# Kernel tuning notes

Hardware: AMD Instinct MI355X
Metric: run time of the kernel (lower is better)

Reference implementation:

```python
import jax, jax.numpy as jnp
import numpy as np

K, B, S, D, V, H = 4, 64, 50, 256, 40000, 4
DH = D // H
TOPK = 2
NEG = -1e9
SCALE = float(1.0 / np.sqrt(DH))


def setup_inputs() -> dict:
    key = jax.random.key(0)
    ks = jax.random.split(key, 16)
    s = 0.05
    return {
        "ids":   jax.random.randint(ks[0], (K, B, S), 0, V),
        "items": jax.random.randint(ks[1], (K, B, S), 0, V),
        "adj":   jax.random.randint(ks[2], (B, S, S), 0, 5),
        "alias": jax.random.randint(ks[3], (B, S), 0, S),
        "eps":   jax.random.normal(ks[4], (B, S, K), jnp.float32),
        "emb":   jax.random.normal(ks[5], (K, V, D), jnp.float32) * s,
        "agg_a": jax.random.normal(ks[6], (K, 4, D), jnp.float32) * s,
        "Wq": jax.random.normal(ks[7], (K, D, D), jnp.float32) * s,
        "Wk": jax.random.normal(ks[8], (K, D, D), jnp.float32) * s,
        "Wv": jax.random.normal(ks[9], (K, D, D), jnp.float32) * s,
        "Wo": jax.random.normal(ks[10], (K, D, D), jnp.float32) * s,
        "ln1_g": jnp.ones((K, D), jnp.float32),
        "ln1_b": jnp.zeros((K, D), jnp.float32),
        "W1": jax.random.normal(ks[11], (K, D, 4 * D), jnp.float32) * s,
        "W2": jax.random.normal(ks[12], (K, 4 * D, D), jnp.float32) * s,
        "ln2_g": jnp.ones((K, D), jnp.float32),
        "ln2_b": jnp.zeros((K, D), jnp.float32),
        "Wg": jax.random.normal(ks[13], (D, K), jnp.float32) * s,
        "Wn": jax.random.normal(ks[14], (D, K), jnp.float32) * s,
    }


def _layer_norm(x, g, b):
    m = jnp.mean(x, -1, keepdims=True)
    v = jnp.var(x, -1, keepdims=True)
    return (x - m) * jax.lax.rsqrt(v + 1e-5) * g + b


def _per_key(ids, items, emb, a, Wq, Wk, Wv, Wo, g1, b1, W1, W2, g2, b2, adj, alias):
    hg = emb[items]                                          # [B,S,D] graph-node embeddings
    # LocalAggregator: relation-typed pairwise attention over session graph (adj in {1..4})
    e = jnp.einsum('bid,bjd,rd->rbij', hg, hg, a)            # [4,B,S,S], avoids [B,S,S,D]
    e = jax.nn.leaky_relu(e, 0.2)
    alpha = jnp.full(adj.shape, NEG, e.dtype)
    for r in range(4):
        alpha = jnp.where(adj == r + 1, e[r], alpha)
    alpha = jax.nn.softmax(alpha, -1)
    h_local = jnp.einsum('bij,bjd->bid', alpha, hg)          # graph aggregation
    h = jnp.take_along_axis(h_local, alias[..., None], axis=1)   # distribute graph rows to sequence
    # memory-transformer block (pre-LN causal MHA + FFN)
    x = _layer_norm(h, g1, b1)
    q = (x @ Wq).reshape(B, S, H, DH)
    k = (x @ Wk).reshape(B, S, H, DH)
    v = (x @ Wv).reshape(B, S, H, DH)
    scores = jnp.einsum('bihd,bjhd->bhij', q, k) * SCALE
    causal = jnp.tril(jnp.ones((S, S), bool))
    scores = jnp.where(causal, scores, NEG)
    attn = jax.nn.softmax(scores, -1)
    o = jnp.einsum('bhij,bjhd->bihd', attn, v).reshape(B, S, D) @ Wo
    h = h + o
    y = _layer_norm(h, g2, b2)
    h = h + jax.nn.gelu(y @ W1) @ W2
    return h


def reference(ids, items, adj, alias, eps, emb, agg_a, Wq, Wk, Wv, Wo,
              ln1_g, ln1_b, W1, W2, ln2_g, ln2_b, Wg, Wn):
    per_key = jax.vmap(_per_key, in_axes=(0,) * 14 + (None, None))
    h_keys = per_key(ids, items, emb, agg_a, Wq, Wk, Wv, Wo,
                     ln1_g, ln1_b, W1, W2, ln2_g, ln2_b, adj, alias)   # [K,B,S,D]
    # gate input: mean over per-key input-sequence embeddings (h_seq in original)
    h_seq = jax.vmap(lambda e, i: e[i])(emb, ids).mean(0)              # [B,S,D]
    # noisy top-k gating over node-type experts
    logits = h_seq @ Wg + jax.nn.softplus(h_seq @ Wn) * eps            # [B,S,K]
    top_v, top_i = jax.lax.top_k(logits, TOPK)
    w = jax.nn.softmax(top_v, -1)                                      # [B,S,TOPK]
    gates = jnp.sum(jax.nn.one_hot(top_i, K, dtype=w.dtype) * w[..., None], axis=-2)  # [B,S,K]
    return jnp.einsum('bsk,kbsd->bsd', gates, h_keys)
```

## Files before the change

### kernel.cpp

```cpp
#include <hip/hip_runtime.h>
#include <hip/hip_bf16.h>
#include <math.h>

#define K_ 4
#define B_ 64
#define S_ 50
#define D_ 256
#define V_ 40000
#define H_ 4
#define DH_ 64
#define NEG_ (-1e9f)
#define SCALE_ 0.125f

typedef __attribute__((ext_vector_type(8))) __bf16 bf16x8v;
typedef __attribute__((ext_vector_type(4))) float f32x4v;

__device__ __forceinline__ float wred_sum(float v) {
#pragma unroll
  for (int off = 32; off > 0; off >>= 1) v += __shfl_xor(v, off, 64);
  return v;
}
__device__ __forceinline__ float wred_max(float v) {
#pragma unroll
  for (int off = 32; off > 0; off >>= 1) v = fmaxf(v, __shfl_xor(v, off, 64));
  return v;
}
__device__ __forceinline__ float softplusf(float x) {
  return (x > 20.f) ? x : log1pf(expf(x));
}
__device__ __forceinline__ float geluf(float x) {
  const float c = 0.7978845608028654f;
  float x3 = x * x * x;
  return 0.5f * x * (1.f + tanhf(c * (x + 0.044715f * x3)));
}
__device__ __forceinline__ float bf2f(unsigned int u) {
  return __uint_as_float(u << 16);
}
__device__ __forceinline__ unsigned short f2bf(float f) {
  unsigned u = __float_as_uint(f);
  return (unsigned short)((u + 0x7fffu + ((u >> 16) & 1u)) >> 16);
}
__device__ __forceinline__ void unp8(uint4 a, float* d) {
  d[0] = bf2f(a.x & 0xffffu); d[1] = bf2f(a.x >> 16);
  d[2] = bf2f(a.y & 0xffffu); d[3] = bf2f(a.y >> 16);
  d[4] = bf2f(a.z & 0xffffu); d[5] = bf2f(a.z >> 16);
  d[6] = bf2f(a.w & 0xffffu); d[7] = bf2f(a.w >> 16);
}
__device__ __forceinline__ bf16x8v cvt8(float4 a, float4 b) {
  bf16x8v r;
  r[0] = (__bf16)a.x; r[1] = (__bf16)a.y; r[2] = (__bf16)a.z; r[3] = (__bf16)a.w;
  r[4] = (__bf16)b.x; r[5] = (__bf16)b.y; r[6] = (__bf16)b.z; r[7] = (__bf16)b.w;
  return r;
}

__global__ __launch_bounds__(256) void cast_weights(
    const float* __restrict__ wq, const float* __restrict__ wk,
    const float* __restrict__ wv, const float* __restrict__ wo,
    const float* __restrict__ w1, const float* __restrict__ w2,
    unsigned short* __restrict__ wqkvT, unsigned short* __restrict__ woT,
    unsigned short* __restrict__ w1T, unsigned short* __restrict__ w2T) {
  long i4 = ((long)blockIdx.x * 256 + threadIdx.x) * 4;
  if (i4 < 786432) {
    int sect = (int)(i4 / 262144);
    long e = i4 - (long)sect * 262144;
    const float* src = (sect == 0) ? wq : (sect == 1) ? wk : wv;
    int k = (int)(e >> 16), rem = (int)(e & 65535);
    int d = rem >> 8, n = rem & 255;
    float4 v = *(const float4*)(src + e);
    unsigned short* base = wqkvT + ((long)k * 768 + sect * 256 + n) * 256 + d;
    base[0] = f2bf(v.x); base[256] = f2bf(v.y);
    base[512] = f2bf(v.z); base[768] = f2bf(v.w);
    return;
  }
  if (i4 < 1048576) {
    long e = i4 - 786432;
    int k = (int)(e >> 16), rem = (int)(e & 65535);
    int d = rem >> 8, n = rem & 255;
    float4 v = *(const float4*)(wo + e);
    unsigned short* base = woT + ((long)k * 256 + n) * 256 + d;
    base[0] = f2bf(v.x); base[256] = f2bf(v.y);
    base[512] = f2bf(v.z); base[768] = f2bf(v.w);
    return;
  }
  if (i4 < 2097152) {
    long e = i4 - 1048576;
    int k = (int)(e >> 18), rem = (int)(e & 262143);
    int d = rem >> 10, n = rem & 1023;
    float4 v = *(const float4*)(w1 + e);
    unsigned short* base = w1T + ((long)k * 1024 + n) * 256 + d;
    base[0] = f2bf(v.x); base[256] = f2bf(v.y);
    base[512] = f2bf(v.z); base[768] = f2bf(v.w);
    return;
  }
  {
    long e = i4 - 2097152;
    int k = (int)(e >> 18), rem = (int)(e & 262143);
    int d = rem >> 8, n = rem & 255;
    float4 v = *(const float4*)(w2 + e);
    unsigned short* base = w2T + ((long)k * 256 + n) * 1024 + d;
    base[0] = f2bf(v.x); base[1024] = f2bf(v.y);
    base[2048] = f2bf(v.z); base[3072] = f2bf(v.w);
  }
}

__global__ __launch_bounds__(256) void gate_kernel(
    const int* __restrict__ ids, const float* __restrict__ emb,
    const float* __restrict__ Wg, const float* __restrict__ Wn,
    const float* __restrict__ eps, float* __restrict__ gates) {
  int w = threadIdx.x >> 6, lane = threadIdx.x & 63;
  int item = blockIdx.x * 4 + w;
  int b = item / S_, s = item % S_;
  int d0 = lane * 4;
  float4 hs = make_float4(0.f, 0.f, 0.f, 0.f);
#pragma unroll
  for (int k = 0; k < K_; ++k) {
    int id = ids[(k * B_ + b) * S_ + s];
    const float4 e = *(const float4*)(emb + ((long)k * V_ + id) * D_ + d0);
    hs.x += e.x; hs.y += e.y; hs.z += e.z; hs.w += e.w;
  }
  hs.x *= 0.25f; hs.y *= 0.25f; hs.z *= 0.25f; hs.w *= 0.25f;
  float logit[4];
#pragma unroll
  for (int j = 0; j < K_; ++j) {
    float pg = hs.x * Wg[(d0 + 0) * K_ + j] + hs.y * Wg[(d0 + 1) * K_ + j] +
               hs.z * Wg[(d0 + 2) * K_ + j] + hs.w * Wg[(d0 + 3) * K_ + j];
    float pn = hs.x * Wn[(d0 + 0) * K_ + j] + hs.y * Wn[(d0 + 1) * K_ + j] +
               hs.z * Wn[(d0 + 2) * K_ + j] + hs.w * Wn[(d0 + 3) * K_ + j];
    pg = wred_sum(pg);
    pn = wred_sum(pn);
    logit[j] = pg + softplusf(pn) * eps[item * K_ + j];
  }
  if (lane == 0) {
    int i0 = 0; float v0 = logit[0];
    for (int j = 1; j < K_; ++j) if (logit[j] > v0) { v0 = logit[j]; i0 = j; }
    int i1 = -1; float v1 = 0.f;
    for (int j = 0; j < K_; ++j)
      if (j != i0 && (i1 < 0 || logit[j] > v1)) { v1 = logit[j]; i1 = j; }
    float w0 = 1.f / (1.f + expf(v1 - v0));
    float w1 = 1.f - w0;
#pragma unroll
    for (int j = 0; j < K_; ++j)
      gates[item * K_ + j] = (j == i0) ? w0 : ((j == i1) ? w1 : 0.f);
  }
}

__global__ __launch_bounds__(256) void local_agg4(
    const int* __restrict__ items, const int* __restrict__ adj,
    const float* __restrict__ emb, const float* __restrict__ agg_a,
    float* __restrict__ h_raw) {
  __shared__ __bf16 hgb[64][264];
  __shared__ float e_f[50][68];
  __shared__ __bf16 alp[64][72];
  __shared__ unsigned char adj_s[64][64];
  __shared__ __bf16 a_sb[4][264];
  int kb = blockIdx.x;
  int k = kb >> 6, b = kb & 63;
  int t = threadIdx.x;
  for (int c = t; c < 2048; c += 256) {
    int row = c >> 5, c8 = (c & 31) * 8;
    bf16x8v val;
    if (row < S_) {
      int g = items[kb * S_ + row];
      const float* src = emb + ((long)k * V_ + g) * D_ + c8;
      val = cvt8(*(const float4*)src, *(const float4*)(src + 4));
    } else {
#pragma unroll
      for (int e = 0; e < 8; ++e) val[e] = (__bf16)0.f;
    }
    *(bf16x8v*)&hgb[row][c8] = val;
  }
  if (t < 128) {
    int row = t >> 5, c8 = (t & 31) * 8;
    const float* src = agg_a + ((long)k * 4 + row) * D_ + c8;
    *(bf16x8v*)&a_sb[row][c8] = cvt8(*(const float4*)src, *(const float4*)(src + 4));
  }
  for (int c = t; c < 4096; c += 256) {
    int i = c >> 6, j = c & 63;
    adj_s[i][j] = (i < S_ && j < S_)
                      ? (unsigned char)adj[((long)b * S_ + i) * S_ + j] : 0;
  }
  __syncthreads();
  int w = t >> 6, lane = t & 63;
  int m16 = lane & 15, quad = lane >> 4;
  float e_sel[4][4];
#pragma unroll
  for (int nt = 0; nt < 4; ++nt)
#pragma unroll
    for (int rg = 0; rg < 4; ++rg) e_sel[nt][rg] = NEG_;
#pragma unroll
  for (int r = 0; r < 4; ++r) {
    f32x4v acc[4];
#pragma unroll
    for (int nt = 0; nt < 4; ++nt) acc[nt] = (f32x4v){0.f, 0.f, 0.f, 0.f};
#pragma unroll
    for (int k0 = 0; k0 < 8; ++k0) {
      int kc = k0 * 32 + quad * 8;
      bf16x8v hr = *(const bf16x8v*)&hgb[w * 16 + m16][kc];
      bf16x8v ar = *(const bf16x8v*)&a_sb[r][kc];
      bf16x8v af;
#pragma unroll
      for (int e = 0; e < 8; ++e) af[e] = (__bf16)((float)hr[e] * (float)ar[e]);
#pragma unroll
      for (int nt = 0; nt < 4; ++nt) {
        bf16x8v bf = *(const bf16x8v*)&hgb[nt * 16 + m16][kc];
        acc[nt] = __builtin_amdgcn_mfma_f32_16x16x32_bf16(af, bf, acc[nt], 0, 0, 0);
      }
    }
#pragma unroll
    for (int nt = 0; nt < 4; ++nt)
#pragma unroll
      for (int rg = 0; rg < 4; ++rg) {
        int i = w * 16 + quad * 4 + rg, j = nt * 16 + m16;
        if (adj_s[i][j] == r + 1) {
          float v = acc[nt][rg];
          e_sel[nt][rg] = (v >= 0.f) ? v : 0.2f * v;
        }
      }
  }
#pragma unroll
  for (int nt = 0; nt < 4; ++nt)
#pragma unroll
    for (int rg = 0; rg < 4; ++rg) {
      int i = w * 16 + quad * 4 + rg;
      if (i < S_) e_f[i][nt * 16 + m16] = e_sel[nt][rg];
    }
  __syncthreads();
  for (int i = w; i < S_; i += 4) {
    float val = (lane < S_) ? e_f[i][lane] : -INFINITY;
    float m = wred_max(val);
    float p = expf(val - m);
    float ssum = wred_sum(p);
    alp[i][lane] = (__bf16)(p / ssum);
  }
  __syncthreads();
#pragma unroll 4
  for (int nt = 0; nt < 16; ++nt) {
    f32x4v acc = (f32x4v){0.f, 0.f, 0.f, 0.f};
#pragma unroll
    for (int k0 = 0; k0 < 2; ++k0) {
      int jb = k0 * 32 + quad * 8;
      bf16x8v af = *(const bf16x8v*)&alp[w * 16 + m16][jb];
      bf16x8v bf;
#pragma unroll
      for (int tt = 0; tt < 8; ++tt) bf[tt] = hgb[jb + tt][nt * 16 + m16];
      acc = __builtin_amdgcn_mfma_f32_16x16x32_bf16(af, bf, acc, 0, 0, 0);
    }
#pragma unroll
    for (int rg = 0; rg < 4; ++rg) {
      int i = w * 16 + quad * 4 + rg;
      if (i < S_)
        h_raw[((long)kb * S_ + i) * D_ + nt * 16 + m16] = acc[rg];
    }
  }
}

__global__ __launch_bounds__(256) void gather_ln(
    const float* __restrict__ h_raw, const int* __restrict__ alias_,
    float* __restrict__ hbuf, unsigned short* __restrict__ xb,
    const float* __restrict__ g, const float* __restrict__ bta) {
  int kb = blockIdx.x;
  int k = kb >> 6, b = kb & 63;
  int w = threadIdx.x >> 6, lane = threadIdx.x & 63;
  for (int s = w; s < S_; s += 4) {
    int src = alias_[b * S_ + s];
    const float4 v = *(const float4*)(h_raw + ((long)kb * S_ + src) * D_ + lane * 4);
    long off = ((long)kb * S_ + s) * D_ + lane * 4;
    *(float4*)(hbuf + off) = v;
    float sum = wred_sum(v.x + v.y + v.z + v.w);
    float sq = wred_sum(v.x * v.x + v.y * v.y + v.z * v.z + v.w * v.w);
    float mean = sum * (1.f / D_);
    float var = sq * (1.f / D_) - mean * mean;
    float rs = rsqrtf(var + 1e-5f);
    const float4 gv = *(const float4*)(g + k * D_ + lane * 4);
    const float4 bv = *(const float4*)(bta + k * D_ + lane * 4);
    ushort4 o;
    o.x = f2bf((v.x - mean) * rs * gv.x + bv.x);
    o.y = f2bf((v.y - mean) * rs * gv.y + bv.y);
    o.z = f2bf((v.z - mean) * rs * gv.z + bv.z);
    o.w = f2bf((v.w - mean) * rs * gv.w + bv.w);
    *(ushort4*)(xb + off) = o;
  }
}

__global__ __launch_bounds__(256) void ln_bf16(
    const float* __restrict__ x, unsigned short* __restrict__ y,
    const float* __restrict__ g, const float* __restrict__ bta) {
  int w = threadIdx.x >> 6, lane = threadIdx.x & 63;
  long row = (long)blockIdx.x * 4 + w;
  int k = (int)(row / (B_ * S_));
  const float4 v = *(const float4*)(x + row * D_ + lane * 4);
  float sum = wred_sum(v.x + v.y + v.z + v.w);
  float sq = wred_sum(v.x * v.x + v.y * v.y + v.z * v.z + v.w * v.w);
  float mean = sum * (1.f / D_);
  float var = sq * (1.f / D_) - mean * mean;
  float rs = rsqrtf(var + 1e-5f);
  const float4 gv = *(const float4*)(g + k * D_ + lane * 4);
  const float4 bv = *(const float4*)(bta + k * D_ + lane * 4);
  ushort4 o;
  o.x = f2bf((v.x - mean) * rs * gv.x + bv.x);
  o.y = f2bf((v.y - mean) * rs * gv.y + bv.y);
  o.z = f2bf((v.z - mean) * rs * gv.z + bv.z);
  o.w = f2bf((v.w - mean) * rs * gv.w + bv.w);
  *(ushort4*)(y + row * D_ + lane * 4) = o;
}

__global__ __launch_bounds__(256) void bgemm2(
    const unsigned short* __restrict__ A, const unsigned short* __restrict__ Bt,
    long strideA, long strideBt, int N, int Kd,
    float* __restrict__ Cf, long strideCf,
    const float* __restrict__ R, long strideR,
    unsigned short* __restrict__ Cb, long strideCb, int act) {
  __shared__ unsigned short sA[64][72];
  __shared__ unsigned short sB[64][72];
  int z = blockIdx.z;
  A += (long)z * strideA;
  Bt += (long)z * strideBt;
  int t = threadIdx.x, w = t >> 6, lane = t & 63;
  int row0 = blockIdx.x * 64, col0 = blockIdx.y * 64;
  int m16 = lane & 15, quad = lane >> 4;
  f32x4v acc[4];
#pragma unroll
  for (int nt = 0; nt < 4; ++nt) acc[nt] = (f32x4v){0.f, 0.f, 0.f, 0.f};
  int sr = t >> 2, sc = (t & 3) * 16;
  const unsigned short* pa = A + (long)(row0 + sr) * Kd + sc;
  const unsigned short* pb = Bt + (long)(col0 + sr) * Kd + sc;
  uint4 a0 = *(const uint4*)(pa);
  uint4 a1 = *(const uint4*)(pa + 8);
  uint4 b0 = *(const uint4*)(pb);
  uint4 b1 = *(const uint4*)(pb + 8);
  for (int k0 = 0; k0 < Kd; k0 += 64) {
    __syncthreads();
    *(uint4*)&sA[sr][sc] = a0;
    *(uint4*)&sA[sr][sc + 8] = a1;
    *(uint4*)&sB[sr][sc] = b0;
    *(uint4*)&sB[sr][sc + 8] = b1;
    if (k0 + 64 < Kd) {
      a0 = *(const uint4*)(pa + k0 + 64);
      a1 = *(const uint4*)(pa + k0 + 72);
      b0 = *(const uint4*)(pb + k0 + 64);
      b1 = *(const uint4*)(pb + k0 + 72);
    }
    __syncthreads();
#pragma unroll
    for (int half = 0; half < 2; ++half) {
      int kg = half * 32 + quad * 8;
      bf16x8v af = *(const bf16x8v*)&sA[w * 16 + m16][kg];
#pragma unroll
      for (int nt = 0; nt < 4; ++nt) {
        bf16x8v bf = *(const bf16x8v*)&sB[nt * 16 + m16][kg];
        acc[nt] = __builtin_amdgcn_mfma_f32_16x16x32_bf16(af, bf, acc[nt], 0, 0, 0);
      }
    }
  }
  int rbase = row0 + w * 16 + quad * 4;
  int cb = m16;
#pragma unroll
  for (int nt = 0; nt < 4; ++nt) {
#pragma unroll
    for (int i2 = 0; i2 < 4; ++i2) {
      long off = (long)(rbase + i2) * N + col0 + nt * 16 + cb;
      float vv = acc[nt][i2];
      if (R) vv += R[(long)z * strideR + off];
      if (act == 1) vv = geluf(vv);
      if (Cf) Cf[(long)z * strideCf + off] = vv;
      if (Cb) Cb[(long)z * strideCb + off] = f2bf(vv);
    }
  }
}

__global__ __launch_bounds__(256) void attn_kernel(
    const unsigned short* __restrict__ qkv, unsigned short* __restrict__ o) {
  __shared__ float qs[S_][65], ks[S_][65], vs[S_][65];
  int idx = blockIdx.x;
  int h = idx & 3;
  int kb = idx >> 2;
  long base = (long)kb * S_ * 768;
  int t = threadIdx.x;
  for (int f = t; f < S_ * 8; f += 256) {
    int row = f >> 3, c8 = (f & 7) * 8;
    long g = base + (long)row * 768 + h * DH_ + c8;
    unp8(*(const uint4*)(qkv + g), &qs[row][c8]);
    unp8(*(const uint4*)(qkv + g + 256), &ks[row][c8]);
    unp8(*(const uint4*)(qkv + g + 512), &vs[row][c8]);
  }
  __syncthreads();
  int w = t >> 6, lane = t & 63;
  for (int i = w; i < S_; i += 4) {
    int jj = (lane < S_) ? lane : 0;
    float dot = 0.f;
#pragma unroll
    for (int d = 0; d < DH_; ++d) dot = fmaf(qs[i][d], ks[jj][d], dot);
    float val = (lane <= i) ? dot * SCALE_ : ((lane < S_) ? NEG_ : -INFINITY);
    float m = wred_max(val);
    float p = expf(val - m);
    float ssum = wred_sum(p);
    float pr = p / ssum;
    float acc = 0.f;
    for (int j = 0; j <= i; ++j)
      acc = fmaf(__shfl(pr, j, 64), vs[j][lane], acc);
    o[((long)kb * S_ + i) * D_ + h * DH_ + lane] = f2bf(acc);
  }
}

__global__ __launch_bounds__(256) void combine_kernel(
    const float* __restrict__ gates, const float* __restrict__ h,
    float* __restrict__ out) {
  int w = threadIdx.x >> 6, lane = threadIdx.x & 63;
  int item = blockIdx.x * 4 + w;
  float g0 = gates[item * 4 + 0], g1 = gates[item * 4 + 1];
  float g2 = gates[item * 4 + 2], g3 = gates[item * 4 + 3];
  long off = (long)item * D_ + lane * 4;
  const long PK = (long)B_ * S_ * D_;
  float4 a = *(const float4*)(h + off);
  float4 b = *(const float4*)(h + PK + off);
  float4 c = *(const float4*)(h + 2 * PK + off);
  float4 d = *(const float4*)(h + 3 * PK + off);
  float4 o;
  o.x = g0 * a.x + g1 * b.x + g2 * c.x + g3 * d.x;
  o.y = g0 * a.y + g1 * b.y + g2 * c.y + g3 * d.y;
  o.z = g0 * a.z + g1 * b.z + g2 * c.z + g3 * d.z;
  o.w = g0 * a.w + g1 * b.w + g2 * c.w + g3 * d.w;
  *(float4*)(out + off) = o;
}

extern "C" void kernel_launch(void* const* d_in, const int* in_sizes, int n_in,
                              void* d_out, int out_size, void* d_ws,
                              size_t ws_size, hipStream_t stream) {
  const int* ids = (const int*)d_in[0];
  const int* items = (const int*)d_in[1];
  const int* adj = (const int*)d_in[2];
  const int* alias = (const int*)d_in[3];
  const float* eps = (const float*)d_in[4];
  const float* emb = (const float*)d_in[5];
  const float* agg_a = (const float*)d_in[6];
  const float* Wq = (const float*)d_in[7];
  const float* Wk = (const float*)d_in[8];
  const float* Wv = (const float*)d_in[9];
  const float* Wo = (const float*)d_in[10];
  const float* ln1g = (const float*)d_in[11];
  const float* ln1b = (const float*)d_in[12];
  const float* W1 = (const float*)d_in[13];
  const float* W2 = (const float*)d_in[14];
  const float* ln2g = (const float*)d_in[15];
  const float* ln2b = (const float*)d_in[16];
  const float* Wg = (const float*)d_in[17];
  const float* Wn = (const float*)d_in[18];
  float* out = (float*)d_out;

  const long BSD = (long)B_ * S_ * D_;
  float* ws = (float*)d_ws;
  float* gates = ws;
  float* hbuf = ws + 16384;
  unsigned short* ub = (unsigned short*)(ws + 16384 + 4 * BSD);
  unsigned short* xb = ub;
  unsigned short* qkvb = ub + 3276800;
  unsigned short* tb = qkvb;
  float* h_raw = (float*)qkvb;
  unsigned short* wqkvT = ub + 16384000;
  unsigned short* woT = wqkvT + 786432;
  unsigned short* w1T = woT + 262144;
  unsigned short* w2T = w1T + 1048576;

  const long T4 = 3276800;

  cast_weights<<<3072, 256, 0, stream>>>(Wq, Wk, Wv, Wo, W1, W2,
                                         wqkvT, woT, w1T, w2T);
  gate_kernel<<<800, 256, 0, stream>>>(ids, emb, Wg, Wn, eps, gates);
  local_agg4<<<256, 256, 0, stream>>>(items, adj, emb, agg_a, h_raw);
  gather_ln<<<256, 256, 0, stream>>>(h_raw, alias, hbuf, xb, ln1g, ln1b);
  bgemm2<<<dim3(50, 12, 4), 256, 0, stream>>>(xb, wqkvT, BSD, 196608, 768, 256,
      (float*)0, 0, (const float*)0, 0, qkvb, 2457600, 0);
  attn_kernel<<<K_ * B_ * H_, 256, 0, stream>>>(qkvb, xb);
  bgemm2<<<dim3(50, 4, 4), 256, 0, stream>>>(xb, woT, BSD, 65536, 256, 256,
      hbuf, BSD, hbuf, BSD, (unsigned short*)0, 0, 0);
  ln_bf16<<<3200, 256, 0, stream>>>(hbuf, xb, ln2g, ln2b);
  bgemm2<<<dim3(50, 16, 4), 256, 0, stream>>>(xb, w1T, BSD, 262144, 1024, 256,
      (float*)0, 0, (const float*)0, 0, tb, T4, 1);
  bgemm2<<<dim3(50, 4, 4), 256, 0, stream>>>(tb, w2T, T4, 262144, 256, 1024,
      hbuf, BSD, hbuf, BSD, (unsigned short*)0, 0, 0);
  combine_kernel<<<800, 256, 0, stream>>>(gates, hbuf, out);
}
```

Measured before the change: 439.0 us.

## Fuse front kernels, Wo GEMM with LayerNorm, and W2 GEMM with gating combine

Merges weight casting, gating and local aggregation into one multi-role front kernel. The weight transpose now goes through an LDS tile, so the bf16 stores are coalesced. The Wo projection is fused with the residual add and the second LayerNorm. The W2 GEMM now loops over the four experts and applies the gates directly, which removes the separate ln_bf16 and combine launches and their HBM round trips. The trade-off is fewer blocks (200) for the fused GEMMs, each doing more serial work, which may lower occupancy and parallelism.

```diff
diff --git a/kernel.cpp b/kernel.cpp
--- a/kernel.cpp
+++ b/kernel.cpp
@@ -53,203 +53,216 @@
   return r;
 }
 
-__global__ __launch_bounds__(256) void cast_weights(
+__global__ __launch_bounds__(256) void front_kernel(
+    const int* __restrict__ items, const int* __restrict__ adj,
+    const float* __restrict__ emb, const float* __restrict__ agg_a,
+    float* __restrict__ h_raw,
+    const int* __restrict__ ids, const float* __restrict__ Wg,
+    const float* __restrict__ Wn, const float* __restrict__ eps,
+    float* __restrict__ gates,
     const float* __restrict__ wq, const float* __restrict__ wk,
     const float* __restrict__ wv, const float* __restrict__ wo,
     const float* __restrict__ w1, const float* __restrict__ w2,
     unsigned short* __restrict__ wqkvT, unsigned short* __restrict__ woT,
     unsigned short* __restrict__ w1T, unsigned short* __restrict__ w2T) {
-  long i4 = ((long)blockIdx.x * 256 + threadIdx.x) * 4;
-  if (i4 < 786432) {
-    int sect = (int)(i4 / 262144);
-    long e = i4 - (long)sect * 262144;
-    const float* src = (sect == 0) ? wq : (sect == 1) ? wk : wv;
-    int k = (int)(e >> 16), rem = (int)(e & 65535);
-    int d = rem >> 8, n = rem & 255;
-    float4 v = *(const float4*)(src + e);
-    unsigned short* base = wqkvT + ((long)k * 768 + sect * 256 + n) * 256 + d;
-    base[0] = f2bf(v.x); base[256] = f2bf(v.y);
-    base[512] = f2bf(v.z); base[768] = f2bf(v.w);
-    return;
-  }
-  if (i4 < 1048576) {
-    long e = i4 - 786432;
-    int k = (int)(e >> 16), rem = (int)(e & 65535);
-    int d = rem >> 8, n = rem & 255;
-    float4 v = *(const float4*)(wo + e);
-    unsigned short* base = woT + ((long)k * 256 + n) * 256 + d;
-    base[0] = f2bf(v.x); base[256] = f2bf(v.y);
-    base[512] = f2bf(v.z); base[768] = f2bf(v.w);
-    return;
-  }
-  if (i4 < 2097152) {
-    long e = i4 - 1048576;
-    int k = (int)(e >> 18), rem = (int)(e & 262143);
-    int d = rem >> 10, n = rem & 1023;
-    float4 v = *(const float4*)(w1 + e);
-    unsigned short* base = w1T + ((long)k * 1024 + n) * 256 + d;
-    base[0] = f2bf(v.x); base[256] = f2bf(v.y);
-    base[512] = f2bf(v.z); base[768] = f2bf(v.w);
-    return;
-  }
-  {
-    long e = i4 - 2097152;
-    int k = (int)(e >> 18), rem = (int)(e & 262143);
-    int d = rem >> 8, n = rem & 255;
-    float4 v = *(const float4*)(w2 + e);
-    unsigned short* base = w2T + ((long)k * 256 + n) * 1024 + d;
-    base[0] = f2bf(v.x); base[1024] = f2bf(v.y);
-    base[2048] = f2bf(v.z); base[3072] = f2bf(v.w);
-  }
-}
-
-__global__ __launch_bounds__(256) void gate_kernel(
-    const int* __restrict__ ids, const float* __restrict__ emb,
-    const float* __restrict__ Wg, const float* __restrict__ Wn,
-    const float* __restrict__ eps, float* __restrict__ gates) {
-  int w = threadIdx.x >> 6, lane = threadIdx.x & 63;
-  int item = blockIdx.x * 4 + w;
-  int b = item / S_, s = item % S_;
-  int d0 = lane * 4;
-  float4 hs = make_float4(0.f, 0.f, 0.f, 0.f);
-#pragma unroll
-  for (int k = 0; k < K_; ++k) {
-    int id = ids[(k * B_ + b) * S_ + s];
-    const float4 e = *(const float4*)(emb + ((long)k * V_ + id) * D_ + d0);
-    hs.x += e.x; hs.y += e.y; hs.z += e.z; hs.w += e.w;
-  }
-  hs.x *= 0.25f; hs.y *= 0.25f; hs.z *= 0.25f; hs.w *= 0.25f;
-  float logit[4];
-#pragma unroll
-  for (int j = 0; j < K_; ++j) {
-    float pg = hs.x * Wg[(d0 + 0) * K_ + j] + hs.y * Wg[(d0 + 1) * K_ + j] +
-               hs.z * Wg[(d0 + 2) * K_ + j] + hs.w * Wg[(d0 + 3) * K_ + j];
-    float pn = hs.x * Wn[(d0 + 0) * K_ + j] + hs.y * Wn[(d0 + 1) * K_ + j] +
-               hs.z * Wn[(d0 + 2) * K_ + j] + hs.w * Wn[(d0 + 3) * K_ + j];
-    pg = wred_sum(pg);
-    pn = wred_sum(pn);
-    logit[j] = pg + softplusf(pn) * eps[item * K_ + j];
-  }
-  if (lane == 0) {
-    int i0 = 0; float v0 = logit[0];
-    for (int j = 1; j < K_; ++j) if (logit[j] > v0) { v0 = logit[j]; i0 = j; }
-    int i1 = -1; float v1 = 0.f;
-    for (int j = 0; j < K_; ++j)
-      if (j != i0 && (i1 < 0 || logit[j] > v1)) { v1 = logit[j]; i1 = j; }
-    float w0 = 1.f / (1.f + expf(v1 - v0));
-    float w1 = 1.f - w0;
-#pragma unroll
-    for (int j = 0; j < K_; ++j)
-      gates[item * K_ + j] = (j == i0) ? w0 : ((j == i1) ? w1 : 0.f);
-  }
-}
-
-__global__ __launch_bounds__(256) void local_agg4(
-    const int* __restrict__ items, const int* __restrict__ adj,
-    const float* __restrict__ emb, const float* __restrict__ agg_a,
-    float* __restrict__ h_raw) {
   __shared__ __bf16 hgb[64][264];
   __shared__ float e_f[50][68];
   __shared__ __bf16 alp[64][72];
   __shared__ unsigned char adj_s[64][64];
   __shared__ __bf16 a_sb[4][264];
-  int kb = blockIdx.x;
-  int k = kb >> 6, b = kb & 63;
+  int bid = blockIdx.x;
   int t = threadIdx.x;
-  for (int c = t; c < 2048; c += 256) {
-    int row = c >> 5, c8 = (c & 31) * 8;
-    bf16x8v val;
-    if (row < S_) {
-      int g = items[kb * S_ + row];
-      const float* src = emb + ((long)k * V_ + g) * D_ + c8;
-      val = cvt8(*(const float4*)src, *(const float4*)(src + 4));
+
+  if (bid < 256) {
+    int kb = bid;
+    int k = kb >> 6, b = kb & 63;
+    for (int c = t; c < 2048; c += 256) {
+      int row = c >> 5, c8 = (c & 31) * 8;
+      bf16x8v val;
+      if (row < S_) {
+        int g = items[kb * S_ + row];
+        const float* src = emb + ((long)k * V_ + g) * D_ + c8;
+        val = cvt8(*(const float4*)src, *(const float4*)(src + 4));
+      } else {
+#pragma unroll
+        for (int e = 0; e < 8; ++e) val[e] = (__bf16)0.f;
+      }
+      *(bf16x8v*)&hgb[row][c8] = val;
+    }
+    if (t < 128) {
+      int row = t >> 5, c8 = (t & 31) * 8;
+      const float* src = agg_a + ((long)k * 4 + row) * D_ + c8;
+      *(bf16x8v*)&a_sb[row][c8] = cvt8(*(const float4*)src, *(const float4*)(src + 4));
+    }
+    for (int c = t; c < 4096; c += 256) {
+      int i = c >> 6, j = c & 63;
+      adj_s[i][j] = (i < S_ && j < S_)
+                        ? (unsigned char)adj[((long)b * S_ + i) * S_ + j] : 0;
+    }
+    __syncthreads();
+    int w = t >> 6, lane = t & 63;
+    int m16 = lane & 15, quad = lane >> 4;
+    float e_sel[4][4];
+#pragma unroll
+    for (int nt = 0; nt < 4; ++nt)
+#pragma unroll
+      for (int rg = 0; rg < 4; ++rg) e_sel[nt][rg] = NEG_;
+#pragma unroll
+    for (int r = 0; r < 4; ++r) {
+      f32x4v acc[4];
+#pragma unroll
+      for (int nt = 0; nt < 4; ++nt) acc[nt] = (f32x4v){0.f, 0.f, 0.f, 0.f};
+#pragma unroll
+      for (int k0 = 0; k0 < 8; ++k0) {
+        int kc = k0 * 32 + quad * 8;
+        bf16x8v hr = *(const bf16x8v*)&hgb[w * 16 + m16][kc];
+        bf16x8v ar = *(const bf16x8v*)&a_sb[r][kc];
+        bf16x8v af;
+#pragma unroll
+        for (int e = 0; e < 8; ++e) af[e] = (__bf16)((float)hr[e] * (float)ar[e]);
+#pragma unroll
+        for (int nt = 0; nt < 4; ++nt) {
+          bf16x8v bf = *(const bf16x8v*)&hgb[nt * 16 + m16][kc];
+          acc[nt] = __builtin_amdgcn_mfma_f32_16x16x32_bf16(af, bf, acc[nt], 0, 0, 0);
+        }
+      }
+#pragma unroll
+      for (int nt = 0; nt < 4; ++nt)
+#pragma unroll
+        for (int rg = 0; rg < 4; ++rg) {
+          int i = w * 16 + quad * 4 + rg, j = nt * 16 + m16;
+          if (adj_s[i][j] == r + 1) {
+            float v = acc[nt][rg];
+            e_sel[nt][rg] = (v >= 0.f) ? v : 0.2f * v;
+          }
+        }
+    }
+#pragma unroll
+    for (int nt = 0; nt < 4; ++nt)
+#pragma unroll
+      for (int rg = 0; rg < 4; ++rg) {
+        int i = w * 16 + quad * 4 + rg;
+        if (i < S_) e_f[i][nt * 16 + m16] = e_sel[nt][rg];
+      }
+    __syncthreads();
+    for (int i = w; i < S_; i += 4) {
+      float val = (lane < S_) ? e_f[i][lane] : -INFINITY;
+      float m = wred_max(val);
+      float p = expf(val - m);
+      float ssum = wred_sum(p);
+      alp[i][lane] = (__bf16)(p / ssum);
+    }
+    __syncthreads();
+#pragma unroll 4
+    for (int nt = 0; nt < 16; ++nt) {
+      f32x4v acc = (f32x4v){0.f, 0.f, 0.f, 0.f};
+#pragma unroll
+      for (int k0 = 0; k0 < 2; ++k0) {
+        int jb = k0 * 32 + quad * 8;
+        bf16x8v af = *(const bf16x8v*)&alp[w * 16 + m16][jb];
+        bf16x8v bf;
+#pragma unroll
+        for (int tt = 0; tt < 8; ++tt) bf[tt] = hgb[jb + tt][nt * 16 + m16];
+        acc = __builtin_amdgcn_mfma_f32_16x16x32_bf16(af, bf, acc, 0, 0, 0);
+      }
+#pragma unroll
+      for (int rg = 0; rg < 4; ++rg) {
+        int i = w * 16 + quad * 4 + rg;
+        if (i < S_)
+          h_raw[((long)kb * S_ + i) * D_ + nt * 16 + m16] = acc[rg];
+      }
+    }
+    return;
+  }
+
+  if (bid < 1024) {
+    int tid = bid - 256;
+    typedef unsigned short row66[66];
+    row66* tile = (row66*)&hgb[0][0];
+    const float* src; unsigned short* dst; int C, R; int r0, c0;
+    if (tid < 192) {
+      int sect = tid >> 6; int rem = tid & 63;
+      int k = rem >> 4, t2 = rem & 15;
+      r0 = (t2 >> 2) * 64; c0 = (t2 & 3) * 64;
+      src = ((sect == 0) ? wq : (sect == 1) ? wk : wv) + (long)k * 65536;
+      dst = wqkvT + ((long)k * 768 + sect * 256) * 256;
+      R = 256; C = 256;
+    } else if (tid < 256) {
+      int rem = tid - 192; int k = rem >> 4, t2 = rem & 15;
+      r0 = (t2 >> 2) * 64; c0 = (t2 & 3) * 64;
+      src = wo + (long)k * 65536; dst = woT + (long)k * 65536;
+      R = 256; C = 256;
+    } else if (tid < 512) {
+      int rem = tid - 256; int k = rem >> 6, t2 = rem & 63;
+      r0 = (t2 >> 4) * 64; c0 = (t2 & 15) * 64;
+      src = w1 + (long)k * 262144; dst = w1T + (long)k * 262144;
+      R = 256; C = 1024;
     } else {
-#pragma unroll
-      for (int e = 0; e < 8; ++e) val[e] = (__bf16)0.f;
-    }
-    *(bf16x8v*)&hgb[row][c8] = val;
-  }
-  if (t < 128) {
-    int row = t >> 5, c8 = (t & 31) * 8;
-    const float* src = agg_a + ((long)k * 4 + row) * D_ + c8;
-    *(bf16x8v*)&a_sb[row][c8] = cvt8(*(const float4*)src, *(const float4*)(src + 4));
-  }
-  for (int c = t; c < 4096; c += 256) {
-    int i = c >> 6, j = c & 63;
-    adj_s[i][j] = (i < S_ && j < S_)
-                      ? (unsigned char)adj[((long)b * S_ + i) * S_ + j] : 0;
-  }
-  __syncthreads();
-  int w = t >> 6, lane = t & 63;
-  int m16 = lane & 15, quad = lane >> 4;
-  float e_sel[4][4];
-#pragma unroll
-  for (int nt = 0; nt < 4; ++nt)
-#pragma unroll
-    for (int rg = 0; rg < 4; ++rg) e_sel[nt][rg] = NEG_;
-#pragma unroll
-  for (int r = 0; r < 4; ++r) {
-    f32x4v acc[4];
-#pragma unroll
-    for (int nt = 0; nt < 4; ++nt) acc[nt] = (f32x4v){0.f, 0.f, 0.f, 0.f};
-#pragma unroll
-    for (int k0 = 0; k0 < 8; ++k0) {
-      int kc = k0 * 32 + quad * 8;
-      bf16x8v hr = *(const bf16x8v*)&hgb[w * 16 + m16][kc];
-      bf16x8v ar = *(const bf16x8v*)&a_sb[r][kc];
-      bf16x8v af;
-#pragma unroll
-      for (int e = 0; e < 8; ++e) af[e] = (__bf16)((float)hr[e] * (float)ar[e]);
-#pragma unroll
-      for (int nt = 0; nt < 4; ++nt) {
-        bf16x8v bf = *(const bf16x8v*)&hgb[nt * 16 + m16][kc];
-        acc[nt] = __builtin_amdgcn_mfma_f32_16x16x32_bf16(af, bf, acc[nt], 0, 0, 0);
-      }
-    }
-#pragma unroll
-    for (int nt = 0; nt < 4; ++nt)
-#pragma unroll
-      for (int rg = 0; rg < 4; ++rg) {
-        int i = w * 16 + quad * 4 + rg, j = nt * 16 + m16;
-        if (adj_s[i][j] == r + 1) {
-          float v = acc[nt][rg];
-          e_sel[nt][rg] = (v >= 0.f) ? v : 0.2f * v;
-        }
-      }
-  }
-#pragma unroll
-  for (int nt = 0; nt < 4; ++nt)
-#pragma unroll
-    for (int rg = 0; rg < 4; ++rg) {
-      int i = w * 16 + quad * 4 + rg;
-      if (i < S_) e_f[i][nt * 16 + m16] = e_sel[nt][rg];
-    }
-  __syncthreads();
-  for (int i = w; i < S_; i += 4) {
-    float val = (lane < S_) ? e_f[i][lane] : -INFINITY;
-    float m = wred_max(val);
-    float p = expf(val - m);
-    float ssum = wred_sum(p);
-    alp[i][lane] = (__bf16)(p / ssum);
-  }
-  __syncthreads();
-#pragma unroll 4
-  for (int nt = 0; nt < 16; ++nt) {
-    f32x4v acc = (f32x4v){0.f, 0.f, 0.f, 0.f};
-#pragma unroll
-    for (int k0 = 0; k0 < 2; ++k0) {
-      int jb = k0 * 32 + quad * 8;
-      bf16x8v af = *(const bf16x8v*)&alp[w * 16 + m16][jb];
-      bf16x8v bf;
-#pragma unroll
-      for (int tt = 0; tt < 8; ++tt) bf[tt] = hgb[jb + tt][nt * 16 + m16];
-      acc = __builtin_amdgcn_mfma_f32_16x16x32_bf16(af, bf, acc, 0, 0, 0);
-    }
-#pragma unroll
-    for (int rg = 0; rg < 4; ++rg) {
-      int i = w * 16 + quad * 4 + rg;
-      if (i < S_)
-        h_raw[((long)kb * S_ + i) * D_ + nt * 16 + m16] = acc[rg];
+      int rem = tid - 512; int k = rem >> 6, t2 = rem & 63;
+      r0 = (t2 >> 2) * 64; c0 = (t2 & 3) * 64;
+      src = w2 + (long)k * 262144; dst = w2T + (long)k * 262144;
+      R = 1024; C = 256;
+    }
+    int sr = t >> 2, sc = (t & 3) * 16;
+    const float* p = src + (long)(r0 + sr) * C + c0 + sc;
+#pragma unroll
+    for (int q = 0; q < 4; ++q) {
+      float4 f = *(const float4*)(p + q * 4);
+      tile[sr][sc + q * 4 + 0] = f2bf(f.x);
+      tile[sr][sc + q * 4 + 1] = f2bf(f.y);
+      tile[sr][sc + q * 4 + 2] = f2bf(f.z);
+      tile[sr][sc + q * 4 + 3] = f2bf(f.w);
+    }
+    __syncthreads();
+    int dc = t >> 2, ch = (t & 3) * 16;
+    unsigned int wds[8];
+#pragma unroll
+    for (int i = 0; i < 8; ++i)
+      wds[i] = (unsigned int)tile[ch + 2 * i][dc] |
+               ((unsigned int)tile[ch + 2 * i + 1][dc] << 16);
+    unsigned short* dp = dst + (long)(c0 + dc) * R + r0 + ch;
+    uint4 o0 = make_uint4(wds[0], wds[1], wds[2], wds[3]);
+    uint4 o1 = make_uint4(wds[4], wds[5], wds[6], wds[7]);
+    *(uint4*)dp = o0;
+    *(uint4*)(dp + 8) = o1;
+    return;
+  }
+
+  {
+    int w = t >> 6, lane = t & 63;
+    int item = (bid - 1024) * 4 + w;
+    int b = item / S_, s = item % S_;
+    int d0 = lane * 4;
+    float4 hs = make_float4(0.f, 0.f, 0.f, 0.f);
+#pragma unroll
+    for (int k = 0; k < K_; ++k) {
+      int id = ids[(k * B_ + b) * S_ + s];
+      const float4 e = *(const float4*)(emb + ((long)k * V_ + id) * D_ + d0);
+      hs.x += e.x; hs.y += e.y; hs.z += e.z; hs.w += e.w;
+    }
+    hs.x *= 0.25f; hs.y *= 0.25f; hs.z *= 0.25f; hs.w *= 0.25f;
+    float logit[4];
+#pragma unroll
+    for (int j = 0; j < K_; ++j) {
+      float pg = hs.x * Wg[(d0 + 0) * K_ + j] + hs.y * Wg[(d0 + 1) * K_ + j] +
+                 hs.z * Wg[(d0 + 2) * K_ + j] + hs.w * Wg[(d0 + 3) * K_ + j];
+      float pn = hs.x * Wn[(d0 + 0) * K_ + j] + hs.y * Wn[(d0 + 1) * K_ + j] +
+                 hs.z * Wn[(d0 + 2) * K_ + j] + hs.w * Wn[(d0 + 3) * K_ + j];
+      pg = wred_sum(pg);
+      pn = wred_sum(pn);
+      logit[j] = pg + softplusf(pn) * eps[item * K_ + j];
+    }
+    if (lane == 0) {
+      int i0 = 0; float v0 = logit[0];
+      for (int j = 1; j < K_; ++j) if (logit[j] > v0) { v0 = logit[j]; i0 = j; }
+      int i1 = -1; float v1 = 0.f;
+      for (int j = 0; j < K_; ++j)
+        if (j != i0 && (i1 < 0 || logit[j] > v1)) { v1 = logit[j]; i1 = j; }
+      float w0 = 1.f / (1.f + expf(v1 - v0));
+      float w1 = 1.f - w0;
+#pragma unroll
+      for (int j = 0; j < K_; ++j)
+        gates[item * K_ + j] = (j == i0) ? w0 : ((j == i1) ? w1 : 0.f);
     }
   }
 }
@@ -282,28 +295,6 @@
   }
 }
 
-__global__ __launch_bounds__(256) void ln_bf16(
-    const float* __restrict__ x, unsigned short* __restrict__ y,
-    const float* __restrict__ g, const float* __restrict__ bta) {
-  int w = threadIdx.x >> 6, lane = threadIdx.x & 63;
-  long row = (long)blockIdx.x * 4 + w;
-  int k = (int)(row / (B_ * S_));
-  const float4 v = *(const float4*)(x + row * D_ + lane * 4);
-  float sum = wred_sum(v.x + v.y + v.z + v.w);
-  float sq = wred_sum(v.x * v.x + v.y * v.y + v.z * v.z + v.w * v.w);
-  float mean = sum * (1.f / D_);
-  float var = sq * (1.f / D_) - mean * mean;
-  float rs = rsqrtf(var + 1e-5f);
-  const float4 gv = *(const float4*)(g + k * D_ + lane * 4);
-  const float4 bv = *(const float4*)(bta + k * D_ + lane * 4);
-  ushort4 o;
-  o.x = f2bf((v.x - mean) * rs * gv.x + bv.x);
-  o.y = f2bf((v.y - mean) * rs * gv.y + bv.y);
-  o.z = f2bf((v.z - mean) * rs * gv.z + bv.z);
-  o.w = f2bf((v.w - mean) * rs * gv.w + bv.w);
-  *(ushort4*)(y + row * D_ + lane * 4) = o;
-}
-
 __global__ __launch_bounds__(256) void bgemm2(
     const unsigned short* __restrict__ A, const unsigned short* __restrict__ Bt,
     long strideA, long strideBt, int N, int Kd,
@@ -402,25 +393,172 @@
   }
 }
 
-__global__ __launch_bounds__(256) void combine_kernel(
-    const float* __restrict__ gates, const float* __restrict__ h,
+__global__ __launch_bounds__(256) void bgemm_oln(
+    const unsigned short* __restrict__ A, const unsigned short* __restrict__ Bt,
+    float* __restrict__ hbuf, unsigned short* __restrict__ y,
+    const float* __restrict__ g2, const float* __restrict__ b2) {
+  __shared__ unsigned short sA[64][72];
+  __shared__ unsigned short sB[256][72];
+  const long BSD = (long)B_ * S_ * D_;
+  int z = blockIdx.z;
+  const unsigned short* Ap = A + (long)z * BSD;
+  const unsigned short* Bp = Bt + (long)z * 65536;
+  int t = threadIdx.x, w = t >> 6, lane = t & 63;
+  int row0 = blockIdx.x * 64;
+  int m16 = lane & 15, quad = lane >> 4;
+  f32x4v acc[16];
+#pragma unroll
+  for (int nt = 0; nt < 16; ++nt) acc[nt] = (f32x4v){0.f, 0.f, 0.f, 0.f};
+  int sr = t >> 2, sc = (t & 3) * 16;
+  const unsigned short* pa = Ap + (long)(row0 + sr) * 256 + sc;
+  const unsigned short* pb = Bp + (long)sr * 256 + sc;
+  uint4 a0 = *(const uint4*)pa;
+  uint4 a1 = *(const uint4*)(pa + 8);
+  uint4 bv[8];
+#pragma unroll
+  for (int q = 0; q < 4; ++q) {
+    bv[2 * q] = *(const uint4*)(pb + q * 16384);
+    bv[2 * q + 1] = *(const uint4*)(pb + q * 16384 + 8);
+  }
+  for (int k0 = 0; k0 < 256; k0 += 64) {
+    __syncthreads();
+    *(uint4*)&sA[sr][sc] = a0;
+    *(uint4*)&sA[sr][sc + 8] = a1;
+#pragma unroll
+    for (int q = 0; q < 4; ++q) {
+      *(uint4*)&sB[q * 64 + sr][sc] = bv[2 * q];
+      *(uint4*)&sB[q * 64 + sr][sc + 8] = bv[2 * q + 1];
+    }
+    if (k0 + 64 < 256) {
+      a0 = *(const uint4*)(pa + k0 + 64);
+      a1 = *(const uint4*)(pa + k0 + 72);
+#pragma unroll
+      for (int q = 0; q < 4; ++q) {
+        bv[2 * q] = *(const uint4*)(pb + q * 16384 + k0 + 64);
+        bv[2 * q + 1] = *(const uint4*)(pb + q * 16384 + k0 + 72);
+      }
+    }
+    __syncthreads();
+#pragma unroll
+    for (int half = 0; half < 2; ++half) {
+      int kg = half * 32 + quad * 8;
+      bf16x8v af = *(const bf16x8v*)&sA[w * 16 + m16][kg];
+#pragma unroll
+      for (int nt = 0; nt < 16; ++nt) {
+        bf16x8v bf = *(const bf16x8v*)&sB[nt * 16 + m16][kg];
+        acc[nt] = __builtin_amdgcn_mfma_f32_16x16x32_bf16(af, bf, acc[nt], 0, 0, 0);
+      }
+    }
+  }
+  long zoff = (long)z * BSD;
+  int rbase = row0 + w * 16 + quad * 4;
+#pragma unroll
+  for (int nt = 0; nt < 16; ++nt)
+#pragma unroll
+    for (int i2 = 0; i2 < 4; ++i2) {
+      long off = zoff + (long)(rbase + i2) * 256 + nt * 16 + m16;
+      float vv = acc[nt][i2] + hbuf[off];
+      acc[nt][i2] = vv;
+      hbuf[off] = vv;
+    }
+  float mean[4], rstd[4];
+#pragma unroll
+  for (int i2 = 0; i2 < 4; ++i2) {
+    float s = 0.f, q = 0.f;
+#pragma unroll
+    for (int nt = 0; nt < 16; ++nt) {
+      float vv = acc[nt][i2];
+      s += vv; q += vv * vv;
+    }
+#pragma unroll
+    for (int off = 1; off < 16; off <<= 1) {
+      s += __shfl_xor(s, off, 64);
+      q += __shfl_xor(q, off, 64);
+    }
+    float m = s * (1.f / D_);
+    float var = q * (1.f / D_) - m * m;
+    mean[i2] = m;
+    rstd[i2] = rsqrtf(var + 1e-5f);
+  }
+#pragma unroll
+  for (int nt = 0; nt < 16; ++nt) {
+    float gv = g2[z * D_ + nt * 16 + m16];
+    float bvv = b2[z * D_ + nt * 16 + m16];
+#pragma unroll
+    for (int i2 = 0; i2 < 4; ++i2) {
+      long off = zoff + (long)(rbase + i2) * 256 + nt * 16 + m16;
+      y[off] = f2bf((acc[nt][i2] - mean[i2]) * rstd[i2] * gv + bvv);
+    }
+  }
+}
+
+__global__ __launch_bounds__(256) void bgemm_f2c(
+    const unsigned short* __restrict__ A, const unsigned short* __restrict__ Bt,
+    const float* __restrict__ hbuf, const float* __restrict__ gates,
     float* __restrict__ out) {
-  int w = threadIdx.x >> 6, lane = threadIdx.x & 63;
-  int item = blockIdx.x * 4 + w;
-  float g0 = gates[item * 4 + 0], g1 = gates[item * 4 + 1];
-  float g2 = gates[item * 4 + 2], g3 = gates[item * 4 + 3];
-  long off = (long)item * D_ + lane * 4;
-  const long PK = (long)B_ * S_ * D_;
-  float4 a = *(const float4*)(h + off);
-  float4 b = *(const float4*)(h + PK + off);
-  float4 c = *(const float4*)(h + 2 * PK + off);
-  float4 d = *(const float4*)(h + 3 * PK + off);
-  float4 o;
-  o.x = g0 * a.x + g1 * b.x + g2 * c.x + g3 * d.x;
-  o.y = g0 * a.y + g1 * b.y + g2 * c.y + g3 * d.y;
-  o.z = g0 * a.z + g1 * b.z + g2 * c.z + g3 * d.z;
-  o.w = g0 * a.w + g1 * b.w + g2 * c.w + g3 * d.w;
-  *(float4*)(out + off) = o;
+  __shared__ unsigned short sA[64][72];
+  __shared__ unsigned short sB[64][72];
+  const long T4 = 3276800;
+  const long BSD = (long)B_ * S_ * D_;
+  int t = threadIdx.x, w = t >> 6, lane = t & 63;
+  int row0 = blockIdx.x * 64, col0 = blockIdx.y * 64;
+  int m16 = lane & 15, quad = lane >> 4;
+  int rbase = row0 + w * 16 + quad * 4;
+  float racc[4][4];
+#pragma unroll
+  for (int nt = 0; nt < 4; ++nt)
+#pragma unroll
+    for (int i2 = 0; i2 < 4; ++i2) racc[nt][i2] = 0.f;
+  int sr = t >> 2, sc = (t & 3) * 16;
+  for (int z = 0; z < K_; ++z) {
+    const unsigned short* pa = A + (long)z * T4 + (long)(row0 + sr) * 1024 + sc;
+    const unsigned short* pb = Bt + (long)z * 262144 + (long)(col0 + sr) * 1024 + sc;
+    f32x4v acc[4];
+#pragma unroll
+    for (int nt = 0; nt < 4; ++nt) acc[nt] = (f32x4v){0.f, 0.f, 0.f, 0.f};
+    uint4 a0 = *(const uint4*)pa;
+    uint4 a1 = *(const uint4*)(pa + 8);
+    uint4 b0 = *(const uint4*)pb;
+    uint4 b1 = *(const uint4*)(pb + 8);
+    for (int k0 = 0; k0 < 1024; k0 += 64) {
+      __syncthreads();
+      *(uint4*)&sA[sr][sc] = a0;
+      *(uint4*)&sA[sr][sc + 8] = a1;
+      *(uint4*)&sB[sr][sc] = b0;
+      *(uint4*)&sB[sr][sc + 8] = b1;
+      if (k0 + 64 < 1024) {
+        a0 = *(const uint4*)(pa + k0 + 64);
+        a1 = *(const uint4*)(pa + k0 + 72);
+        b0 = *(const uint4*)(pb + k0 + 64);
+        b1 = *(const uint4*)(pb + k0 + 72);
+      }
+      __syncthreads();
+#pragma unroll
+      for (int half = 0; half < 2; ++half) {
+        int kg = half * 32 + quad * 8;
+        bf16x8v af = *(const bf16x8v*)&sA[w * 16 + m16][kg];
+#pragma unroll
+        for (int nt = 0; nt < 4; ++nt) {
+          bf16x8v bf = *(const bf16x8v*)&sB[nt * 16 + m16][kg];
+          acc[nt] = __builtin_amdgcn_mfma_f32_16x16x32_bf16(af, bf, acc[nt], 0, 0, 0);
+        }
+      }
+    }
+#pragma unroll
+    for (int i2 = 0; i2 < 4; ++i2) {
+      float gz = gates[(rbase + i2) * 4 + z];
+#pragma unroll
+      for (int nt = 0; nt < 4; ++nt) {
+        long off = (long)z * BSD + (long)(rbase + i2) * 256 + col0 + nt * 16 + m16;
+        racc[nt][i2] += gz * (acc[nt][i2] + hbuf[off]);
+      }
+    }
+  }
+#pragma unroll
+  for (int nt = 0; nt < 4; ++nt)
+#pragma unroll
+    for (int i2 = 0; i2 < 4; ++i2)
+      out[(long)(rbase + i2) * 256 + col0 + nt * 16 + m16] = racc[nt][i2];
 }
 
 extern "C" void kernel_launch(void* const* d_in, const int* in_sizes, int n_in,
@@ -463,20 +601,15 @@
 
   const long T4 = 3276800;
 
-  cast_weights<<<3072, 256, 0, stream>>>(Wq, Wk, Wv, Wo, W1, W2,
-                                         wqkvT, woT, w1T, w2T);
-  gate_kernel<<<800, 256, 0, stream>>>(ids, emb, Wg, Wn, eps, gates);
-  local_agg4<<<256, 256, 0, stream>>>(items, adj, emb, agg_a, h_raw);
+  front_kernel<<<1824, 256, 0, stream>>>(
+      items, adj, emb, agg_a, h_raw, ids, Wg, Wn, eps, gates,
+      Wq, Wk, Wv, Wo, W1, W2, wqkvT, woT, w1T, w2T);
   gather_ln<<<256, 256, 0, stream>>>(h_raw, alias, hbuf, xb, ln1g, ln1b);
   bgemm2<<<dim3(50, 12, 4), 256, 0, stream>>>(xb, wqkvT, BSD, 196608, 768, 256,
       (float*)0, 0, (const float*)0, 0, qkvb, 2457600, 0);
   attn_kernel<<<K_ * B_ * H_, 256, 0, stream>>>(qkvb, xb);
-  bgemm2<<<dim3(50, 4, 4), 256, 0, stream>>>(xb, woT, BSD, 65536, 256, 256,
-      hbuf, BSD, hbuf, BSD, (unsigned short*)0, 0, 0);
-  ln_bf16<<<3200, 256, 0, stream>>>(hbuf, xb, ln2g, ln2b);
+  bgemm_oln<<<dim3(50, 1, 4), 256, 0, stream>>>(xb, woT, hbuf, xb, ln2g, ln2b);
   bgemm2<<<dim3(50, 16, 4), 256, 0, stream>>>(xb, w1T, BSD, 262144, 1024, 256,
       (float*)0, 0, (const float*)0, 0, tb, T4, 1);
-  bgemm2<<<dim3(50, 4, 4), 256, 0, stream>>>(tb, w2T, T4, 262144, 256, 1024,
-      hbuf, BSD, hbuf, BSD, (unsigned short*)0, 0, 0);
-  combine_kernel<<<800, 256, 0, stream>>>(gates, hbuf, out);
-}
+  bgemm_f2c<<<dim3(50, 4), 256, 0, stream>>>(tb, w2T, hbuf, gates, out);
+}
```

After: 423.0 us. 1.04x faster.
